# Optimization experiments

Measured on AMD Instinct MI355X. Metric: run time of the kernel, lower is better.

Reference implementation:

```python
import jax, jax.numpy as jnp
import numpy as np

N_HEAD = 8
D_MODEL = 512
D_K = 64
D_V = 64
LN_EPS = 1e-6


def setup_inputs() -> dict:
    key = jax.random.key(0)
    ks = jax.random.split(key, 8)
    B, L = 4, 1024
    inp = {
        "q": jax.random.normal(ks[0], (B, L, D_MODEL), dtype=jnp.float32),
        "k": jax.random.normal(ks[1], (B, L, D_MODEL), dtype=jnp.float32),
        "v": jax.random.normal(ks[2], (B, L, D_MODEL), dtype=jnp.float32),
        "w_qs": jax.random.normal(ks[3], (D_MODEL, N_HEAD * D_K), dtype=jnp.float32) * 0.02,
        "w_ks": jax.random.normal(ks[4], (D_MODEL, N_HEAD * D_K), dtype=jnp.float32) * 0.02,
        "w_vs": jax.random.normal(ks[5], (D_MODEL, N_HEAD * D_V), dtype=jnp.float32) * 0.02,
        "w_sk": jax.random.normal(ks[6], (D_V, N_HEAD * D_V), dtype=jnp.float32) * 0.02,
        "w_fc": jax.random.normal(ks[7], (D_V, D_MODEL), dtype=jnp.float32) * 0.02,
        "ln_gamma": jnp.ones((D_MODEL,), dtype=jnp.float32),
        "ln_beta": jnp.zeros((D_MODEL,), dtype=jnp.float32),
    }
    return inp


def reference(q, k, v, w_qs, w_ks, w_vs, w_sk, w_fc, ln_gamma, ln_beta):
    B, Lq, _ = q.shape
    Lk = k.shape[1]
    temp = jnp.asarray(D_K ** 0.5, q.dtype)
    residual = q

    # QKV projections (bias=False), split heads: [B, H, L, d]
    qh = (q @ w_qs).reshape(B, Lq, N_HEAD, D_K).transpose(0, 2, 1, 3)
    kh = (k @ w_ks).reshape(B, Lk, N_HEAD, D_K).transpose(0, 2, 1, 3)
    vh = (v @ w_vs).reshape(B, Lk, N_HEAD, D_V).transpose(0, 2, 1, 3)

    # scaled dot-product attention (dropout in eval mode = identity)
    attn = jax.nn.softmax(jnp.einsum('bhqd,bhkd->bhqk', qh / temp, kh), axis=-1)
    o = jnp.einsum('bhqk,bhkd->bhqd', attn, vh)  # [B, H, Lq, D_V]

    # SPA: selective parallel attention head gating
    u = o.sum(axis=1)                       # [B, Lq, D_V]
    s = u.mean(axis=1)                      # adaptive avg pool over Lq -> [B, D_V]
    g = jax.nn.softmax((s @ w_sk).reshape(B, N_HEAD, D_V), axis=1)  # softmax over heads
    f = o * g[:, :, None, :]                # gate each head, broadcast over Lq
    qo = f.sum(axis=1)                      # sum heads -> [B, Lq, D_V]

    # fc + residual + LayerNorm (dropout eval = identity)
    out = qo @ w_fc + residual              # [B, Lq, D_MODEL]
    mu = out.mean(axis=-1, keepdims=True)
    var = out.var(axis=-1, keepdims=True)
    out = (out - mu) * jax.lax.rsqrt(var + LN_EPS) * ln_gamma + ln_beta
    return out, attn
```

## Files before the change

### kernel.cpp

```cpp
#include <hip/hip_runtime.h>
#include <hip/hip_bf16.h>
#include <cstdint>

#define NH 8
#define DM 512
#define DH 64
#define NB 4
#define SL 1024

typedef __attribute__((ext_vector_type(8))) short bf16x8;
typedef __attribute__((ext_vector_type(4))) float f32x4;

static __device__ __forceinline__ float bf2f(short s) {
  union { unsigned int u; float f; } c;
  c.u = ((unsigned int)(unsigned short)s) << 16;
  return c.f;
}
static __device__ __forceinline__ unsigned short f2bfbits(float f) {
  union { float f; unsigned int u; } c; c.f = f;
  unsigned int lsb = (c.u >> 16) & 1u;
  unsigned int r = c.u + 0x7fffu + lsb;
  return (unsigned short)(r >> 16);
}

__global__ __launch_bounds__(256) void k_cvt_all(
    const float* __restrict__ q, const float* __restrict__ k, const float* __restrict__ v,
    ushort* __restrict__ qb, ushort* __restrict__ kb, ushort* __restrict__ vb,
    const float* __restrict__ w0, const float* __restrict__ w1, const float* __restrict__ w2,
    ushort* __restrict__ o0, ushort* __restrict__ o1, ushort* __restrict__ o2,
    const float* __restrict__ wfc, ushort* __restrict__ wfcb) {
  __shared__ ushort tile[64][65];
  int b = blockIdx.x, t = threadIdx.x;
  if (b < 2048) {
    int i = b * 256 + t;
    {
      float4 f = ((const float4*)q)[i];
      ushort4 r = { f2bfbits(f.x), f2bfbits(f.y), f2bfbits(f.z), f2bfbits(f.w) };
      *(ushort4*)(qb + 4 * i) = r;
    }
    {
      float4 f = ((const float4*)k)[i];
      ushort4 r = { f2bfbits(f.x), f2bfbits(f.y), f2bfbits(f.z), f2bfbits(f.w) };
      *(ushort4*)(kb + 4 * i) = r;
    }
    {
      float4 f = ((const float4*)v)[i];
      ushort4 r = { f2bfbits(f.x), f2bfbits(f.y), f2bfbits(f.z), f2bfbits(f.w) };
      *(ushort4*)(vb + 4 * i) = r;
    }
  } else if (b < 2240) {
    int idx = b - 2048;
    int z = idx >> 6, rem = idx & 63;
    int k0 = (rem & 7) * 64, n0 = (rem >> 3) * 64;
    const float* src = z == 0 ? w0 : (z == 1 ? w1 : w2);
    ushort* dst = z == 0 ? o0 : (z == 1 ? o1 : o2);
    #pragma unroll
    for (int i = 0; i < 16; ++i) {
      int lin = t + i * 256, r = lin >> 6, c = lin & 63;
      tile[r][c] = f2bfbits(src[(size_t)(k0 + r) * DM + n0 + c]);
    }
    __syncthreads();
    #pragma unroll
    for (int i = 0; i < 16; ++i) {
      int lin = t + i * 256, r = lin >> 6, c = lin & 63;
      dst[(size_t)(n0 + r) * DM + k0 + c] = tile[c][r];
    }
  } else {
    int i = (b - 2240) * 256 + t;
    float4 f = ((const float4*)wfc)[i];
    ushort4 r = { f2bfbits(f.x), f2bfbits(f.y), f2bfbits(f.z), f2bfbits(f.w) };
    *(ushort4*)(wfcb + 4 * i) = r;
  }
}

__global__ __launch_bounds__(256) void k_proj(
    const ushort* __restrict__ qb, const ushort* __restrict__ kb, const ushort* __restrict__ vb,
    const ushort* __restrict__ wqT, const ushort* __restrict__ wkT, const ushort* __restrict__ wvT,
    ushort* __restrict__ Qh, ushort* __restrict__ Kh, ushort* __restrict__ VhT) {
  int z = blockIdx.z;
  const ushort* A = z == 0 ? qb : (z == 1 ? kb : vb);
  const ushort* W = z == 0 ? wqT : (z == 1 ? wkT : wvT);
  ushort* Out = z == 0 ? Qh : (z == 1 ? Kh : VhT);
  float scale = z == 0 ? 0.125f * 1.44269504088896f : 1.0f;

  int wid = threadIdx.x >> 6, l = threadIdx.x & 63;
  int lr = l & 15, lg = l >> 4;
  int row0 = blockIdx.x * 64 + wid * 16;
  int col0 = blockIdx.y * 64;
  const ushort* Arow = A + (size_t)(row0 + lr) * DM + lg * 8;

  f32x4 acc0 = {0.f, 0.f, 0.f, 0.f}, acc1 = acc0, acc2 = acc0, acc3 = acc0;
  #pragma unroll 4
  for (int kt = 0; kt < 16; ++kt) {
    bf16x8 a = *(const bf16x8*)(Arow + kt * 32);
    bf16x8 b0 = *(const bf16x8*)(W + (size_t)(col0 + 0 * 16 + lr) * DM + kt * 32 + lg * 8);
    bf16x8 b1 = *(const bf16x8*)(W + (size_t)(col0 + 1 * 16 + lr) * DM + kt * 32 + lg * 8);
    bf16x8 b2 = *(const bf16x8*)(W + (size_t)(col0 + 2 * 16 + lr) * DM + kt * 32 + lg * 8);
    bf16x8 b3 = *(const bf16x8*)(W + (size_t)(col0 + 3 * 16 + lr) * DM + kt * 32 + lg * 8);
    acc0 = __builtin_amdgcn_mfma_f32_16x16x32_bf16(a, b0, acc0, 0, 0, 0);
    acc1 = __builtin_amdgcn_mfma_f32_16x16x32_bf16(a, b1, acc1, 0, 0, 0);
    acc2 = __builtin_amdgcn_mfma_f32_16x16x32_bf16(a, b2, acc2, 0, 0, 0);
    acc3 = __builtin_amdgcn_mfma_f32_16x16x32_bf16(a, b3, acc3, 0, 0, 0);
  }
  f32x4 accs[4] = {acc0, acc1, acc2, acc3};
  #pragma unroll
  for (int ct = 0; ct < 4; ++ct) {
    int gcol = col0 + ct * 16 + lr;
    int h = gcol >> 6, d = gcol & 63;
    #pragma unroll
    for (int r = 0; r < 4; ++r) {
      int grow = row0 + lg * 4 + r;
      int bb = grow >> 10, li = grow & 1023;
      float val = accs[ct][r] * scale;
      size_t addr;
      if (z == 2) addr = ((size_t)((bb * NH + h) * DH + d)) * SL + li;
      else        addr = ((size_t)((bb * NH + h) * SL + li)) * DH + d;
      Out[addr] = f2bfbits(val);
    }
  }
}

__global__ __launch_bounds__(256, 4) void k_attn(
    const ushort* __restrict__ Qh, const ushort* __restrict__ Kh, const ushort* __restrict__ VhT,
    float* __restrict__ attn_out, float* __restrict__ O) {
  __shared__ __align__(16) ushort S[16 * 1024];
  __shared__ float spart[4][16];
  char* Sb = (char*)S;

  int bid = blockIdx.x;
  int xcd = bid & 7;
  int loc = bid >> 3;
  int bh  = xcd * 4 + (loc >> 6);
  int rt  = loc & 63;
  int wid = threadIdx.x >> 6, l = threadIdx.x & 63;
  int lr = l & 15, g = l >> 4;
  int q0 = rt * 16;

  const ushort* Qbase = Qh + ((size_t)(bh * SL + q0 + lr)) * DH + g * 8;
  bf16x8 bQ0 = *(const bf16x8*)(Qbase);
  bf16x8 bQ1 = *(const bf16x8*)(Qbase + 32);
  const ushort* Kbase = Kh + (size_t)bh * SL * DH + (size_t)lr * DH + g * 8;

  float sacc = 0.f;
  const ushort* kp0 = Kbase + (size_t)(wid * 256) * DH;
  bf16x8 ka0 = *(const bf16x8*)(kp0);
  bf16x8 ka1 = *(const bf16x8*)(kp0 + 32);
  bf16x8 kb0 = *(const bf16x8*)(kp0 + 16 * DH);
  bf16x8 kb1 = *(const bf16x8*)(kp0 + 16 * DH + 32);
  #pragma unroll
  for (int ct = 0; ct < 16; ++ct) {
    bf16x8 c0 = (ct & 1) ? kb0 : ka0;
    bf16x8 c1 = (ct & 1) ? kb1 : ka1;
    if (ct < 14) {
      const ushort* kn = Kbase + (size_t)(wid * 256 + (ct + 2) * 16) * DH;
      if (ct & 1) { kb0 = *(const bf16x8*)(kn); kb1 = *(const bf16x8*)(kn + 32); }
      else        { ka0 = *(const bf16x8*)(kn); ka1 = *(const bf16x8*)(kn + 32); }
    }
    f32x4 acc = {0.f, 0.f, 0.f, 0.f};
    acc = __builtin_amdgcn_mfma_f32_16x16x32_bf16(c0, bQ0, acc, 0, 0, 0);
    acc = __builtin_amdgcn_mfma_f32_16x16x32_bf16(c1, bQ1, acc, 0, 0, 0);
    int k0 = wid * 256 + ct * 16;
    float p0 = exp2f(acc[0]), p1 = exp2f(acc[1]);
    float p2 = exp2f(acc[2]), p3 = exp2f(acc[3]);
    sacc += (p0 + p1) + (p2 + p3);
    unsigned int pk0, pk1;
    asm("v_cvt_pk_bf16_f32 %0, %1, %2" : "=v"(pk0) : "v"(p0), "v"(p1));
    asm("v_cvt_pk_bf16_f32 %0, %1, %2" : "=v"(pk1) : "v"(p2), "v"(p3));
    uint2 w2 = { pk0, pk1 };
    *(uint2*)(Sb + (((lr << 11) + ((k0 + 4 * g) << 1)) ^ ((lr & 7) << 4))) = w2;
  }
  sacc += __shfl_xor(sacc, 16);
  sacc += __shfl_xor(sacc, 32);
  if (l < 16) spart[wid][l] = sacc;
  __syncthreads();

  const ushort* Vbase = VhT + (size_t)bh * DH * SL + (size_t)(wid * 16 + lr) * SL + g * 8;
  size_t attn_base = (size_t)bh * SL * SL + (size_t)q0 * SL;
  f32x4 accA = {0.f, 0.f, 0.f, 0.f}, accB = accA;
  bf16x8 va[16];

  #pragma unroll
  for (int kt = 0; kt < 16; ++kt) va[kt] = *(const bf16x8*)(Vbase + kt * 32);
  #pragma unroll
  for (int kt = 0; kt < 16; ++kt) {
    bf16x8 aP = *(const bf16x8*)(Sb + (((lr << 11) + ((kt * 32 + g * 8) << 1)) ^ ((lr & 7) << 4)));
    if (kt & 1) accB = __builtin_amdgcn_mfma_f32_16x16x32_bf16(aP, va[kt], accB, 0, 0, 0);
    else        accA = __builtin_amdgcn_mfma_f32_16x16x32_bf16(aP, va[kt], accA, 0, 0, 0);
  }
  #pragma unroll
  for (int kt = 0; kt < 16; ++kt) va[kt] = *(const bf16x8*)(Vbase + (16 + kt) * 32);
  #pragma unroll
  for (int j = 0; j < 8; ++j) {
    int rr = j >> 1, i = j & 1;
    int r = wid * 4 + rr;
    float inv = 1.0f / (spart[0][r] + spart[1][r] + spart[2][r] + spart[3][r]);
    int c0 = 4 * l + 256 * i;
    uint2 u = *(uint2*)(Sb + (((r << 11) + (c0 << 1)) ^ ((r & 7) << 4)));
    f32x4 pv;
    pv[0] = bf2f((short)(u.x & 0xffff)) * inv;
    pv[1] = bf2f((short)(u.x >> 16)) * inv;
    pv[2] = bf2f((short)(u.y & 0xffff)) * inv;
    pv[3] = bf2f((short)(u.y >> 16)) * inv;
    __builtin_nontemporal_store(pv, (f32x4*)(attn_out + attn_base + (size_t)r * SL + c0));
  }
  #pragma unroll
  for (int kt = 0; kt < 16; ++kt) {
    bf16x8 aP = *(const bf16x8*)(Sb + (((lr << 11) + (((16 + kt) * 32 + g * 8) << 1)) ^ ((lr & 7) << 4)));
    if (kt & 1) accB = __builtin_amdgcn_mfma_f32_16x16x32_bf16(aP, va[kt], accB, 0, 0, 0);
    else        accA = __builtin_amdgcn_mfma_f32_16x16x32_bf16(aP, va[kt], accA, 0, 0, 0);
  }
  #pragma unroll
  for (int j = 0; j < 8; ++j) {
    int rr = j >> 1, i = 2 + (j & 1);
    int r = wid * 4 + rr;
    float inv = 1.0f / (spart[0][r] + spart[1][r] + spart[2][r] + spart[3][r]);
    int c0 = 4 * l + 256 * i;
    uint2 u = *(uint2*)(Sb + (((r << 11) + (c0 << 1)) ^ ((r & 7) << 4)));
    f32x4 pv;
    pv[0] = bf2f((short)(u.x & 0xffff)) * inv;
    pv[1] = bf2f((short)(u.x >> 16)) * inv;
    pv[2] = bf2f((short)(u.y & 0xffff)) * inv;
    pv[3] = bf2f((short)(u.y >> 16)) * inv;
    __builtin_nontemporal_store(pv, (f32x4*)(attn_out + attn_base + (size_t)r * SL + c0));
  }
  f32x4 acc = accA;
  acc[0] += accB[0]; acc[1] += accB[1]; acc[2] += accB[2]; acc[3] += accB[3];
  #pragma unroll
  for (int r = 0; r < 4; ++r) {
    int qr = 4 * g + r;
    float inv = 1.0f / (spart[0][qr] + spart[1][qr] + spart[2][qr] + spart[3][qr]);
    O[((size_t)(bh * SL + q0 + qr)) * DH + wid * 16 + lr] = acc[r] * inv;
  }
}

__global__ __launch_bounds__(256) void k_reduce(const float* __restrict__ O, float* __restrict__ partial) {
  int slab = blockIdx.x, bb = blockIdx.y;
  int d = threadIdx.x & 63, sub = threadIdx.x >> 6;
  float s = 0.f;
  for (int h = 0; h < NH; ++h) {
    const float* base = O + ((size_t)((bb * NH + h) * SL + slab * 16 + sub * 4)) * DH + d;
    #pragma unroll
    for (int li = 0; li < 4; ++li) s += base[(size_t)li * DH];
  }
  __shared__ float red[4][64];
  red[sub][d] = s;
  __syncthreads();
  if (threadIdx.x < 64) {
    float t = red[0][d] + red[1][d] + red[2][d] + red[3][d];
    partial[(bb * 64 + slab) * 64 + d] = t;
  }
}

__global__ __launch_bounds__(256) void k_gate(const float* __restrict__ partial,
                                              const float* __restrict__ wsk, float* __restrict__ g) {
  int bb = blockIdx.x;
  int t = threadIdx.x;
  __shared__ float red[4][64];
  __shared__ float sl[64];
  __shared__ float logit[512];
  int d = t & 63, q4 = t >> 6;
  float s = 0.f;
  for (int i = 0; i < 16; ++i) s += partial[(bb * 64 + q4 * 16 + i) * 64 + d];
  red[q4][d] = s;
  __syncthreads();
  if (t < 64) sl[t] = (red[0][t] + red[1][t] + red[2][t] + red[3][t]) * (1.0f / 1024.0f);
  __syncthreads();
  #pragma unroll
  for (int jj = 0; jj < 2; ++jj) {
    int j = t + jj * 256;
    float lg = 0.f;
    #pragma unroll 8
    for (int c = 0; c < 64; ++c) lg += sl[c] * wsk[c * DM + j];
    logit[j] = lg;
  }
  __syncthreads();
  if (t < 64) {
    float m = -1e30f;
    #pragma unroll
    for (int h = 0; h < NH; ++h) m = fmaxf(m, logit[h * 64 + t]);
    float sum = 0.f, e[NH];
    #pragma unroll
    for (int h = 0; h < NH; ++h) { e[h] = __expf(logit[h * 64 + t] - m); sum += e[h]; }
    float inv = 1.0f / sum;
    #pragma unroll
    for (int h = 0; h < NH; ++h) g[bb * DM + h * 64 + t] = e[h] * inv;
  }
}

__global__ __launch_bounds__(256) void k_final(
    const float* __restrict__ O, const float* __restrict__ g, const ushort* __restrict__ wfc,
    const float* __restrict__ q, const float* __restrict__ gamma, const float* __restrict__ beta,
    float* __restrict__ out) {
  __shared__ __align__(16) ushort wl[32768];
  __shared__ __align__(16) float qo[16][64];
  __shared__ __align__(16) float gl[512];
  int lt = blockIdx.x, bb = blockIdx.y;
  int t = threadIdx.x;

  gl[t] = g[bb * DM + t];
  gl[t + 256] = g[bb * DM + 256 + t];
  {
    int jg2 = t & 15, hi = t >> 4;
    #pragma unroll
    for (int m = 0; m < 16; ++m) {
      int di = m * 16 + hi;
      int d = di >> 2, i8 = di & 3;
      bf16x8 w8 = *(const bf16x8*)(wfc + d * DM + jg2 * 32 + i8 * 8);
      *(bf16x8*)(wl + (size_t)(d * 64 + i8 * 16 + jg2) * 8) = w8;
    }
  }
  __syncthreads();

  int r = t >> 4, jg = t & 15;
  int l = lt * 16 + r;
  {
    float4 acc; acc.x = acc.y = acc.z = acc.w = 0.f;
    #pragma unroll
    for (int h = 0; h < NH; ++h) {
      float4 ov = *(const float4*)(O + ((size_t)((bb * NH + h) * SL + l)) * DH + jg * 4);
      float4 gv = *(const float4*)(gl + h * 64 + jg * 4);
      acc.x += ov.x * gv.x; acc.y += ov.y * gv.y; acc.z += ov.z * gv.z; acc.w += ov.w * gv.w;
    }
    *(float4*)&qo[r][jg * 4] = acc;
  }
  __syncthreads();

  float val[32];
  const float* qrow = q + ((size_t)(bb * SL + l)) * DM + jg * 32;
  #pragma unroll
  for (int i4 = 0; i4 < 8; ++i4) *(float4*)&val[i4 * 4] = *(const float4*)(qrow + i4 * 4);

  for (int d = 0; d < 64; ++d) {
    float qd = qo[r][d];
    #pragma unroll
    for (int i8 = 0; i8 < 4; ++i8) {
      bf16x8 wv8 = *(const bf16x8*)(wl + (size_t)(d * 64 + i8 * 16 + jg) * 8);
      #pragma unroll
      for (int e = 0; e < 8; ++e) val[i8 * 8 + e] += qd * bf2f(wv8[e]);
    }
  }

  float s = 0.f, ss = 0.f;
  #pragma unroll
  for (int i = 0; i < 32; ++i) { s += val[i]; ss += val[i] * val[i]; }
  #pragma unroll
  for (int m = 1; m < 16; m <<= 1) { s += __shfl_xor(s, m, 16); ss += __shfl_xor(ss, m, 16); }
  float mu = s * (1.0f / 512.0f);
  float var = ss * (1.0f / 512.0f) - mu * mu;
  float rstd = rsqrtf(var + 1e-6f);

  float* orow = out + ((size_t)(bb * SL + l)) * DM + jg * 32;
  const float* gam = gamma + jg * 32;
  const float* bet = beta + jg * 32;
  #pragma unroll
  for (int i = 0; i < 32; ++i)
    orow[i] = (val[i] - mu) * rstd * gam[i] + bet[i];
}

extern "C" void kernel_launch(void* const* d_in, const int* in_sizes, int n_in,
                              void* d_out, int out_size, void* d_ws, size_t ws_size,
                              hipStream_t stream) {
  (void)in_sizes; (void)n_in; (void)out_size; (void)ws_size;
  const float* q     = (const float*)d_in[0];
  const float* k     = (const float*)d_in[1];
  const float* v     = (const float*)d_in[2];
  const float* w_qs  = (const float*)d_in[3];
  const float* w_ks  = (const float*)d_in[4];
  const float* w_vs  = (const float*)d_in[5];
  const float* w_sk  = (const float*)d_in[6];
  const float* w_fc  = (const float*)d_in[7];
  const float* gamma = (const float*)d_in[8];
  const float* beta  = (const float*)d_in[9];

  float* out  = (float*)d_out;
  float* attn = out + (size_t)NB * SL * DM;

  char* wsb = (char*)d_ws;
  ushort* qb   = (ushort*)(wsb + 0);
  ushort* kb   = (ushort*)(wsb + 4194304);
  ushort* vb   = (ushort*)(wsb + 8388608);
  ushort* wqT  = (ushort*)(wsb + 12582912);
  ushort* wkT  = (ushort*)(wsb + 13107200);
  ushort* wvT  = (ushort*)(wsb + 13631488);
  ushort* wfcb = (ushort*)(wsb + 14155776);
  ushort* Qh   = (ushort*)(wsb + 14221312);
  ushort* Kh   = (ushort*)(wsb + 18415616);
  ushort* VhT  = (ushort*)(wsb + 22609920);
  float*  O    = (float*)(wsb + 26804224);
  float*  part = (float*)(wsb + 0);
  float*  gbuf = (float*)(wsb + 65536);

  k_cvt_all<<<dim3(2272), dim3(256), 0, stream>>>(q, k, v, qb, kb, vb,
                                                  w_qs, w_ks, w_vs, wqT, wkT, wvT,
                                                  w_fc, wfcb);
  k_proj<<<dim3(64, 8, 3), dim3(256), 0, stream>>>(qb, kb, vb, wqT, wkT, wvT, Qh, Kh, VhT);
  k_attn<<<dim3(2048), dim3(256), 0, stream>>>(Qh, Kh, VhT, attn, O);
  k_reduce<<<dim3(64, 4), dim3(256), 0, stream>>>(O, part);
  k_gate<<<dim3(4), dim3(256), 0, stream>>>(part, w_sk, gbuf);
  k_final<<<dim3(64, 4), dim3(256), 0, stream>>>(O, gbuf, wfcb, q, gamma, beta, out);
}
```

Baseline: 163.4 us.

## Fuse activation bf16 conversion into projection GEMM and batch attn stores at end

Removes the separate fp32-to-bf16 pass over q, k, v. The projection kernel now loads fp32 activations directly and converts them in registers with v_cvt_pk_bf16_f32, which avoids writing and re-reading 12 MB of bf16 copies. Fp32 reads are doubled and repeated across the 8 column blocks, so that traffic rises. The attention kernel also defers all attn probability stores and the O store to after the final MFMA loop, holding 16 f32x4 in registers. This raises register pressure but no longer interleaves stores with compute.

After: 172.6 us. 5.6% more time.

```diff
diff --git a/kernel.cpp b/kernel.cpp
--- a/kernel.cpp
+++ b/kernel.cpp
@@ -23,34 +23,14 @@
   return (unsigned short)(r >> 16);
 }
 
-__global__ __launch_bounds__(256) void k_cvt_all(
-    const float* __restrict__ q, const float* __restrict__ k, const float* __restrict__ v,
-    ushort* __restrict__ qb, ushort* __restrict__ kb, ushort* __restrict__ vb,
+__global__ __launch_bounds__(256) void k_cvt_w(
     const float* __restrict__ w0, const float* __restrict__ w1, const float* __restrict__ w2,
     ushort* __restrict__ o0, ushort* __restrict__ o1, ushort* __restrict__ o2,
     const float* __restrict__ wfc, ushort* __restrict__ wfcb) {
   __shared__ ushort tile[64][65];
   int b = blockIdx.x, t = threadIdx.x;
-  if (b < 2048) {
-    int i = b * 256 + t;
-    {
-      float4 f = ((const float4*)q)[i];
-      ushort4 r = { f2bfbits(f.x), f2bfbits(f.y), f2bfbits(f.z), f2bfbits(f.w) };
-      *(ushort4*)(qb + 4 * i) = r;
-    }
-    {
-      float4 f = ((const float4*)k)[i];
-      ushort4 r = { f2bfbits(f.x), f2bfbits(f.y), f2bfbits(f.z), f2bfbits(f.w) };
-      *(ushort4*)(kb + 4 * i) = r;
-    }
-    {
-      float4 f = ((const float4*)v)[i];
-      ushort4 r = { f2bfbits(f.x), f2bfbits(f.y), f2bfbits(f.z), f2bfbits(f.w) };
-      *(ushort4*)(vb + 4 * i) = r;
-    }
-  } else if (b < 2240) {
-    int idx = b - 2048;
-    int z = idx >> 6, rem = idx & 63;
+  if (b < 192) {
+    int z = b >> 6, rem = b & 63;
     int k0 = (rem & 7) * 64, n0 = (rem >> 3) * 64;
     const float* src = z == 0 ? w0 : (z == 1 ? w1 : w2);
     ushort* dst = z == 0 ? o0 : (z == 1 ? o1 : o2);
@@ -66,7 +46,7 @@
       dst[(size_t)(n0 + r) * DM + k0 + c] = tile[c][r];
     }
   } else {
-    int i = (b - 2240) * 256 + t;
+    int i = (b - 192) * 256 + t;
     float4 f = ((const float4*)wfc)[i];
     ushort4 r = { f2bfbits(f.x), f2bfbits(f.y), f2bfbits(f.z), f2bfbits(f.w) };
     *(ushort4*)(wfcb + 4 * i) = r;
@@ -74,11 +54,11 @@
 }
 
 __global__ __launch_bounds__(256) void k_proj(
-    const ushort* __restrict__ qb, const ushort* __restrict__ kb, const ushort* __restrict__ vb,
+    const float* __restrict__ qf, const float* __restrict__ kf, const float* __restrict__ vf,
     const ushort* __restrict__ wqT, const ushort* __restrict__ wkT, const ushort* __restrict__ wvT,
     ushort* __restrict__ Qh, ushort* __restrict__ Kh, ushort* __restrict__ VhT) {
   int z = blockIdx.z;
-  const ushort* A = z == 0 ? qb : (z == 1 ? kb : vb);
+  const float* Af = z == 0 ? qf : (z == 1 ? kf : vf);
   const ushort* W = z == 0 ? wqT : (z == 1 ? wkT : wvT);
   ushort* Out = z == 0 ? Qh : (z == 1 ? Kh : VhT);
   float scale = z == 0 ? 0.125f * 1.44269504088896f : 1.0f;
@@ -87,12 +67,19 @@
   int lr = l & 15, lg = l >> 4;
   int row0 = blockIdx.x * 64 + wid * 16;
   int col0 = blockIdx.y * 64;
-  const ushort* Arow = A + (size_t)(row0 + lr) * DM + lg * 8;
+  const float* Arow = Af + (size_t)(row0 + lr) * DM + lg * 8;
 
   f32x4 acc0 = {0.f, 0.f, 0.f, 0.f}, acc1 = acc0, acc2 = acc0, acc3 = acc0;
-  #pragma unroll 4
+  #pragma unroll 2
   for (int kt = 0; kt < 16; ++kt) {
-    bf16x8 a = *(const bf16x8*)(Arow + kt * 32);
+    float4 f0 = *(const float4*)(Arow + kt * 32);
+    float4 f1 = *(const float4*)(Arow + kt * 32 + 4);
+    union { unsigned int u[4]; bf16x8 v; } au;
+    asm("v_cvt_pk_bf16_f32 %0, %1, %2" : "=v"(au.u[0]) : "v"(f0.x), "v"(f0.y));
+    asm("v_cvt_pk_bf16_f32 %0, %1, %2" : "=v"(au.u[1]) : "v"(f0.z), "v"(f0.w));
+    asm("v_cvt_pk_bf16_f32 %0, %1, %2" : "=v"(au.u[2]) : "v"(f1.x), "v"(f1.y));
+    asm("v_cvt_pk_bf16_f32 %0, %1, %2" : "=v"(au.u[3]) : "v"(f1.z), "v"(f1.w));
+    bf16x8 a = au.v;
     bf16x8 b0 = *(const bf16x8*)(W + (size_t)(col0 + 0 * 16 + lr) * DM + kt * 32 + lg * 8);
     bf16x8 b1 = *(const bf16x8*)(W + (size_t)(col0 + 1 * 16 + lr) * DM + kt * 32 + lg * 8);
     bf16x8 b2 = *(const bf16x8*)(W + (size_t)(col0 + 2 * 16 + lr) * DM + kt * 32 + lg * 8);
@@ -190,47 +177,48 @@
   #pragma unroll
   for (int kt = 0; kt < 16; ++kt) va[kt] = *(const bf16x8*)(Vbase + (16 + kt) * 32);
   #pragma unroll
-  for (int j = 0; j < 8; ++j) {
-    int rr = j >> 1, i = j & 1;
-    int r = wid * 4 + rr;
-    float inv = 1.0f / (spart[0][r] + spart[1][r] + spart[2][r] + spart[3][r]);
-    int c0 = 4 * l + 256 * i;
-    uint2 u = *(uint2*)(Sb + (((r << 11) + (c0 << 1)) ^ ((r & 7) << 4)));
-    f32x4 pv;
-    pv[0] = bf2f((short)(u.x & 0xffff)) * inv;
-    pv[1] = bf2f((short)(u.x >> 16)) * inv;
-    pv[2] = bf2f((short)(u.y & 0xffff)) * inv;
-    pv[3] = bf2f((short)(u.y >> 16)) * inv;
-    __builtin_nontemporal_store(pv, (f32x4*)(attn_out + attn_base + (size_t)r * SL + c0));
-  }
-  #pragma unroll
   for (int kt = 0; kt < 16; ++kt) {
     bf16x8 aP = *(const bf16x8*)(Sb + (((lr << 11) + (((16 + kt) * 32 + g * 8) << 1)) ^ ((lr & 7) << 4)));
     if (kt & 1) accB = __builtin_amdgcn_mfma_f32_16x16x32_bf16(aP, va[kt], accB, 0, 0, 0);
     else        accA = __builtin_amdgcn_mfma_f32_16x16x32_bf16(aP, va[kt], accA, 0, 0, 0);
   }
-  #pragma unroll
-  for (int j = 0; j < 8; ++j) {
-    int rr = j >> 1, i = 2 + (j & 1);
+
+  float invs[4];
+  #pragma unroll
+  for (int rr = 0; rr < 4; ++rr) {
     int r = wid * 4 + rr;
-    float inv = 1.0f / (spart[0][r] + spart[1][r] + spart[2][r] + spart[3][r]);
+    invs[rr] = 1.0f / (spart[0][r] + spart[1][r] + spart[2][r] + spart[3][r]);
+  }
+  f32x4 pv[16];
+  #pragma unroll
+  for (int j = 0; j < 16; ++j) {
+    int rr = j >> 2, i = j & 3;
+    int r = wid * 4 + rr;
     int c0 = 4 * l + 256 * i;
     uint2 u = *(uint2*)(Sb + (((r << 11) + (c0 << 1)) ^ ((r & 7) << 4)));
-    f32x4 pv;
-    pv[0] = bf2f((short)(u.x & 0xffff)) * inv;
-    pv[1] = bf2f((short)(u.x >> 16)) * inv;
-    pv[2] = bf2f((short)(u.y & 0xffff)) * inv;
-    pv[3] = bf2f((short)(u.y >> 16)) * inv;
-    __builtin_nontemporal_store(pv, (f32x4*)(attn_out + attn_base + (size_t)r * SL + c0));
-  }
-  f32x4 acc = accA;
-  acc[0] += accB[0]; acc[1] += accB[1]; acc[2] += accB[2]; acc[3] += accB[3];
+    pv[j][0] = bf2f((short)(u.x & 0xffff)) * invs[rr];
+    pv[j][1] = bf2f((short)(u.x >> 16)) * invs[rr];
+    pv[j][2] = bf2f((short)(u.y & 0xffff)) * invs[rr];
+    pv[j][3] = bf2f((short)(u.y >> 16)) * invs[rr];
+  }
+  f32x4 oval = accA;
+  oval[0] += accB[0]; oval[1] += accB[1]; oval[2] += accB[2]; oval[3] += accB[3];
   #pragma unroll
   for (int r = 0; r < 4; ++r) {
     int qr = 4 * g + r;
     float inv = 1.0f / (spart[0][qr] + spart[1][qr] + spart[2][qr] + spart[3][qr]);
-    O[((size_t)(bh * SL + q0 + qr)) * DH + wid * 16 + lr] = acc[r] * inv;
-  }
+    oval[r] *= inv;
+  }
+
+  #pragma unroll
+  for (int j = 0; j < 16; ++j) {
+    int rr = j >> 2, i = j & 3;
+    __builtin_nontemporal_store(pv[j],
+        (f32x4*)(attn_out + attn_base + (size_t)(wid * 4 + rr) * SL + 4 * l + 256 * i));
+  }
+  #pragma unroll
+  for (int r = 0; r < 4; ++r)
+    O[((size_t)(bh * SL + q0 + 4 * g + r)) * DH + wid * 16 + lr] = oval[r];
 }
 
 __global__ __launch_bounds__(256) void k_reduce(const float* __restrict__ O, float* __restrict__ partial) {
@@ -376,9 +364,6 @@
   float* attn = out + (size_t)NB * SL * DM;
 
   char* wsb = (char*)d_ws;
-  ushort* qb   = (ushort*)(wsb + 0);
-  ushort* kb   = (ushort*)(wsb + 4194304);
-  ushort* vb   = (ushort*)(wsb + 8388608);
   ushort* wqT  = (ushort*)(wsb + 12582912);
   ushort* wkT  = (ushort*)(wsb + 13107200);
   ushort* wvT  = (ushort*)(wsb + 13631488);
@@ -390,10 +375,8 @@
   float*  part = (float*)(wsb + 0);
   float*  gbuf = (float*)(wsb + 65536);
 
-  k_cvt_all<<<dim3(2272), dim3(256), 0, stream>>>(q, k, v, qb, kb, vb,
-                                                  w_qs, w_ks, w_vs, wqT, wkT, wvT,
-                                                  w_fc, wfcb);
-  k_proj<<<dim3(64, 8, 3), dim3(256), 0, stream>>>(qb, kb, vb, wqT, wkT, wvT, Qh, Kh, VhT);
+  k_cvt_w<<<dim3(224), dim3(256), 0, stream>>>(w_qs, w_ks, w_vs, wqT, wkT, wvT, w_fc, wfcb);
+  k_proj<<<dim3(64, 8, 3), dim3(256), 0, stream>>>(q, k, v, wqT, wkT, wvT, Qh, Kh, VhT);
   k_attn<<<dim3(2048), dim3(256), 0, stream>>>(Qh, Kh, VhT, attn, O);
   k_reduce<<<dim3(64, 4), dim3(256), 0, stream>>>(O, part);
   k_gate<<<dim3(4), dim3(256), 0, stream>>>(part, w_sk, gbuf);
```

## Fuse fp32-to-bf16 activation conversion into projection GEMM with LDS-staged A tiles

Applied to the files above, without the earlier changes.

Removes the separate conversion pass that wrote bf16 copies of q, k and v. The projection kernel now loads fp32 rows, converts them with packed bf16 conversion instructions into swizzled LDS, and computes a 64x256 output tile per block with 16 accumulators per wave. This saves a full write-and-reread of the activations and reuses each A tile across four times more columns. The cost is 64KB of LDS per block, much higher register pressure, and fewer blocks (384) to fill the GPU.

Result: slower. 170.9 us (+4.6%).

```diff
diff --git a/kernel.cpp b/kernel.cpp
--- a/kernel.cpp
+++ b/kernel.cpp
@@ -10,6 +10,7 @@
 
 typedef __attribute__((ext_vector_type(8))) short bf16x8;
 typedef __attribute__((ext_vector_type(4))) float f32x4;
+typedef __attribute__((ext_vector_type(4))) unsigned int u32x4;
 
 static __device__ __forceinline__ float bf2f(short s) {
   union { unsigned int u; float f; } c;
@@ -23,34 +24,14 @@
   return (unsigned short)(r >> 16);
 }
 
-__global__ __launch_bounds__(256) void k_cvt_all(
-    const float* __restrict__ q, const float* __restrict__ k, const float* __restrict__ v,
-    ushort* __restrict__ qb, ushort* __restrict__ kb, ushort* __restrict__ vb,
+__global__ __launch_bounds__(256) void k_cvt_w(
     const float* __restrict__ w0, const float* __restrict__ w1, const float* __restrict__ w2,
     ushort* __restrict__ o0, ushort* __restrict__ o1, ushort* __restrict__ o2,
     const float* __restrict__ wfc, ushort* __restrict__ wfcb) {
   __shared__ ushort tile[64][65];
   int b = blockIdx.x, t = threadIdx.x;
-  if (b < 2048) {
-    int i = b * 256 + t;
-    {
-      float4 f = ((const float4*)q)[i];
-      ushort4 r = { f2bfbits(f.x), f2bfbits(f.y), f2bfbits(f.z), f2bfbits(f.w) };
-      *(ushort4*)(qb + 4 * i) = r;
-    }
-    {
-      float4 f = ((const float4*)k)[i];
-      ushort4 r = { f2bfbits(f.x), f2bfbits(f.y), f2bfbits(f.z), f2bfbits(f.w) };
-      *(ushort4*)(kb + 4 * i) = r;
-    }
-    {
-      float4 f = ((const float4*)v)[i];
-      ushort4 r = { f2bfbits(f.x), f2bfbits(f.y), f2bfbits(f.z), f2bfbits(f.w) };
-      *(ushort4*)(vb + 4 * i) = r;
-    }
-  } else if (b < 2240) {
-    int idx = b - 2048;
-    int z = idx >> 6, rem = idx & 63;
+  if (b < 192) {
+    int z = b >> 6, rem = b & 63;
     int k0 = (rem & 7) * 64, n0 = (rem >> 3) * 64;
     const float* src = z == 0 ? w0 : (z == 1 ? w1 : w2);
     ushort* dst = z == 0 ? o0 : (z == 1 ? o1 : o2);
@@ -66,7 +47,7 @@
       dst[(size_t)(n0 + r) * DM + k0 + c] = tile[c][r];
     }
   } else {
-    int i = (b - 2240) * 256 + t;
+    int i = (b - 192) * 256 + t;
     float4 f = ((const float4*)wfc)[i];
     ushort4 r = { f2bfbits(f.x), f2bfbits(f.y), f2bfbits(f.z), f2bfbits(f.w) };
     *(ushort4*)(wfcb + 4 * i) = r;
@@ -74,44 +55,64 @@
 }
 
 __global__ __launch_bounds__(256) void k_proj(
-    const ushort* __restrict__ qb, const ushort* __restrict__ kb, const ushort* __restrict__ vb,
+    const float* __restrict__ qf, const float* __restrict__ kf, const float* __restrict__ vf,
     const ushort* __restrict__ wqT, const ushort* __restrict__ wkT, const ushort* __restrict__ wvT,
     ushort* __restrict__ Qh, ushort* __restrict__ Kh, ushort* __restrict__ VhT) {
+  __shared__ __align__(16) ushort Al[64 * 512];
+  char* Ab = (char*)Al;
   int z = blockIdx.z;
-  const ushort* A = z == 0 ? qb : (z == 1 ? kb : vb);
+  const float* Af = z == 0 ? qf : (z == 1 ? kf : vf);
   const ushort* W = z == 0 ? wqT : (z == 1 ? wkT : wvT);
   ushort* Out = z == 0 ? Qh : (z == 1 ? Kh : VhT);
   float scale = z == 0 ? 0.125f * 1.44269504088896f : 1.0f;
 
-  int wid = threadIdx.x >> 6, l = threadIdx.x & 63;
+  int t = threadIdx.x;
+  int row0 = blockIdx.x * 64;
+  int col0 = blockIdx.y * 256;
+
+  const float4* A4 = (const float4*)(Af + (size_t)row0 * DM);
+  #pragma unroll
+  for (int j = 0; j < 16; ++j) {
+    int p = j * 256 + t;
+    float4 f0 = A4[2 * p];
+    float4 f1 = A4[2 * p + 1];
+    union { unsigned int u[4]; u32x4 v; } au;
+    asm("v_cvt_pk_bf16_f32 %0, %1, %2" : "=v"(au.u[0]) : "v"(f0.x), "v"(f0.y));
+    asm("v_cvt_pk_bf16_f32 %0, %1, %2" : "=v"(au.u[1]) : "v"(f0.z), "v"(f0.w));
+    asm("v_cvt_pk_bf16_f32 %0, %1, %2" : "=v"(au.u[2]) : "v"(f1.x), "v"(f1.y));
+    asm("v_cvt_pk_bf16_f32 %0, %1, %2" : "=v"(au.u[3]) : "v"(f1.z), "v"(f1.w));
+    int row = p >> 6, g = p & 63;
+    *(u32x4*)(Ab + (((row << 10) + (g << 4)) ^ ((row & 7) << 4))) = au.v;
+  }
+  __syncthreads();
+
+  int wid = t >> 6, l = t & 63;
   int lr = l & 15, lg = l >> 4;
-  int row0 = blockIdx.x * 64 + wid * 16;
-  int col0 = blockIdx.y * 64;
-  const ushort* Arow = A + (size_t)(row0 + lr) * DM + lg * 8;
-
-  f32x4 acc0 = {0.f, 0.f, 0.f, 0.f}, acc1 = acc0, acc2 = acc0, acc3 = acc0;
-  #pragma unroll 4
+  int brow = wid * 16;
+
+  f32x4 acc[16];
+  #pragma unroll
+  for (int ct = 0; ct < 16; ++ct) acc[ct] = (f32x4){0.f, 0.f, 0.f, 0.f};
+
   for (int kt = 0; kt < 16; ++kt) {
-    bf16x8 a = *(const bf16x8*)(Arow + kt * 32);
-    bf16x8 b0 = *(const bf16x8*)(W + (size_t)(col0 + 0 * 16 + lr) * DM + kt * 32 + lg * 8);
-    bf16x8 b1 = *(const bf16x8*)(W + (size_t)(col0 + 1 * 16 + lr) * DM + kt * 32 + lg * 8);
-    bf16x8 b2 = *(const bf16x8*)(W + (size_t)(col0 + 2 * 16 + lr) * DM + kt * 32 + lg * 8);
-    bf16x8 b3 = *(const bf16x8*)(W + (size_t)(col0 + 3 * 16 + lr) * DM + kt * 32 + lg * 8);
-    acc0 = __builtin_amdgcn_mfma_f32_16x16x32_bf16(a, b0, acc0, 0, 0, 0);
-    acc1 = __builtin_amdgcn_mfma_f32_16x16x32_bf16(a, b1, acc1, 0, 0, 0);
-    acc2 = __builtin_amdgcn_mfma_f32_16x16x32_bf16(a, b2, acc2, 0, 0, 0);
-    acc3 = __builtin_amdgcn_mfma_f32_16x16x32_bf16(a, b3, acc3, 0, 0, 0);
-  }
-  f32x4 accs[4] = {acc0, acc1, acc2, acc3};
-  #pragma unroll
-  for (int ct = 0; ct < 4; ++ct) {
+    int arow = brow + lr;
+    bf16x8 a = *(const bf16x8*)(Ab + (((arow << 10) + kt * 64 + lg * 16) ^ ((arow & 7) << 4)));
+    #pragma unroll
+    for (int ct = 0; ct < 16; ++ct) {
+      bf16x8 b = *(const bf16x8*)(W + (size_t)(col0 + ct * 16 + lr) * DM + kt * 32 + lg * 8);
+      acc[ct] = __builtin_amdgcn_mfma_f32_16x16x32_bf16(a, b, acc[ct], 0, 0, 0);
+    }
+  }
+
+  #pragma unroll
+  for (int ct = 0; ct < 16; ++ct) {
     int gcol = col0 + ct * 16 + lr;
     int h = gcol >> 6, d = gcol & 63;
     #pragma unroll
     for (int r = 0; r < 4; ++r) {
-      int grow = row0 + lg * 4 + r;
+      int grow = row0 + brow + lg * 4 + r;
       int bb = grow >> 10, li = grow & 1023;
-      float val = accs[ct][r] * scale;
+      float val = acc[ct][r] * scale;
       size_t addr;
       if (z == 2) addr = ((size_t)((bb * NH + h) * DH + d)) * SL + li;
       else        addr = ((size_t)((bb * NH + h) * SL + li)) * DH + d;
@@ -376,9 +377,6 @@
   float* attn = out + (size_t)NB * SL * DM;
 
   char* wsb = (char*)d_ws;
-  ushort* qb   = (ushort*)(wsb + 0);
-  ushort* kb   = (ushort*)(wsb + 4194304);
-  ushort* vb   = (ushort*)(wsb + 8388608);
   ushort* wqT  = (ushort*)(wsb + 12582912);
   ushort* wkT  = (ushort*)(wsb + 13107200);
   ushort* wvT  = (ushort*)(wsb + 13631488);
@@ -390,10 +388,8 @@
   float*  part = (float*)(wsb + 0);
   float*  gbuf = (float*)(wsb + 65536);
 
-  k_cvt_all<<<dim3(2272), dim3(256), 0, stream>>>(q, k, v, qb, kb, vb,
-                                                  w_qs, w_ks, w_vs, wqT, wkT, wvT,
-                                                  w_fc, wfcb);
-  k_proj<<<dim3(64, 8, 3), dim3(256), 0, stream>>>(qb, kb, vb, wqT, wkT, wvT, Qh, Kh, VhT);
+  k_cvt_w<<<dim3(224), dim3(256), 0, stream>>>(w_qs, w_ks, w_vs, wqT, wkT, wvT, w_fc, wfcb);
+  k_proj<<<dim3(64, 2, 3), dim3(256), 0, stream>>>(q, k, v, wqT, wkT, wvT, Qh, Kh, VhT);
   k_attn<<<dim3(2048), dim3(256), 0, stream>>>(Qh, Kh, VhT, attn, O);
   k_reduce<<<dim3(64, 4), dim3(256), 0, stream>>>(O, part);
   k_gate<<<dim3(4), dim3(256), 0, stream>>>(part, w_sk, gbuf);
```
